# Kernel tuning notes

Measured on AMD Instinct MI355X. Metric: run time of the kernel, lower is better.

## Reference

```python
import jax, jax.numpy as jnp
import numpy as np

N, K, FEAT = 64, 32, 1024      # nodes, neighbors per node, input feature dim
C1, F1 = 4, 16                 # layer1: out_channels=4, out_features=hidden[0]/4=16
C2, F2 = 32, 1                 # layer2: out_channels=hidden[1]=32, out_features=1
NUM_CLASS = 10
BN_EPS = 1e-5


def _sgnroot(x):
    return jnp.sign(x) * jnp.sqrt(jnp.clip(jnp.abs(x), 1e-8))


def _feature_adjacency(x, nb):
    # x: (N,c,f), nb: (N,K,c,f) -> adj: (N,c,f,f)
    fadj = jnp.einsum('nca,nkcb->ncab', x, nb)          # sum over K neighbors
    fadj = fadj + jnp.swapaxes(fadj, -2, -1)
    s = _sgnroot(fadj)
    out = s / (jnp.abs(s).sum(axis=1, keepdims=True) + 1e-7)  # row-normalize over channel dim
    return jnp.where(jnp.isnan(out), 0.0, out)


def _layer(x, nb, W, c_out, f_out):
    # FeatTrans1d.forward: adjacency build + batched matmul + full-width conv (== dense contraction)
    n = x.shape[0]
    adj = _feature_adjacency(x, nb)                     # (N,c,f,f)
    xa = jnp.einsum('ncab,ncb->nca', adj, x)            # adj @ x
    x2 = jnp.einsum('ocf,ncf->no', W, xa).reshape(n, c_out, f_out)
    na = jnp.einsum('ncab,nkcb->nkca', adj, nb)         # per-node adj applied to its neighbors
    nb2 = jnp.einsum('ocf,nkcf->nko', W, na).reshape(n, -1, c_out, f_out)
    return x2, nb2


def _bn_softsign_x(x, w, b):
    # BatchNorm1d (training stats over batch+feature dims) + Softsign; x: (N,C,F)
    m = x.mean(axis=(0, 2), keepdims=True)
    v = x.var(axis=(0, 2), keepdims=True)
    y = (x - m) / jnp.sqrt(v + BN_EPS) * w[None, :, None] + b[None, :, None]
    return y / (1.0 + jnp.abs(y))


def _bn_softsign_nb(x, w, b):
    # each node's neighbor set is normalized independently (list comprehension in original); x: (N,K,C,F)
    m = x.mean(axis=(1, 3), keepdims=True)
    v = x.var(axis=(1, 3), keepdims=True)
    y = (x - m) / jnp.sqrt(v + BN_EPS) * w[None, None, :, None] + b[None, None, :, None]
    return y / (1.0 + jnp.abs(y))


def setup_inputs() -> dict:
    key = jax.random.key(0)
    ks = jax.random.split(key, 6)
    return {
        'x': jax.random.normal(ks[0], (N, 1, FEAT), jnp.float32),
        'neighbor': jax.random.normal(ks[1], (N, K, 1, FEAT), jnp.float32),
        'W1': jax.random.normal(ks[2], (C1 * F1, 1, FEAT), jnp.float32) * (1.0 / FEAT) ** 0.5,
        'W2': jax.random.normal(ks[3], (C2 * F2, C1, F1), jnp.float32) * (1.0 / (C1 * F1)) ** 0.5,
        'bn1_w': jnp.ones((C1,), jnp.float32),
        'bn1_b': jnp.zeros((C1,), jnp.float32),
        'bn2_w': jnp.ones((C2,), jnp.float32),
        'bn2_b': jnp.zeros((C2,), jnp.float32),
        'lin_w': jax.random.normal(ks[4], (NUM_CLASS, C2 * F2), jnp.float32) * (1.0 / (C2 * F2)) ** 0.5,
        'lin_b': jnp.zeros((NUM_CLASS,), jnp.float32),
    }


def reference(x, neighbor, W1, W2, bn1_w, bn1_b, bn2_w, bn2_b, lin_w, lin_b):
    x1, nb1 = _layer(x, neighbor, W1, C1, F1)           # (N,4,16), (N,K,4,16)
    x1 = _bn_softsign_x(x1, bn1_w, bn1_b)
    nb1 = _bn_softsign_nb(nb1, bn1_w, bn1_b)
    x2, _ = _layer(x1, nb1, W2, C2, F2)                 # (N,32,1)
    x2 = _bn_softsign_x(x2, bn2_w, bn2_b)
    return x2.reshape(x2.shape[0], -1) @ lin_w.T + lin_b  # (N,NUM_CLASS)
```

## Files before the change

kernel.cpp:

```cpp
#include <hip/hip_runtime.h>

typedef unsigned short u16;
typedef short short8 __attribute__((ext_vector_type(8)));
typedef float floatx4 __attribute__((ext_vector_type(4)));
typedef float floatx2 __attribute__((ext_vector_type(2)));
typedef unsigned int uintx4 __attribute__((ext_vector_type(4)));
typedef unsigned int uintx2 __attribute__((ext_vector_type(2)));
typedef u16 ushortx4 __attribute__((ext_vector_type(4)));

#define FEAT 1024
#define KNB  32

__device__ __forceinline__ u16 f2bf(float f) {
    unsigned u = __float_as_uint(f);
    u += 0x7fffu + ((u >> 16) & 1u);
    return (u16)(u >> 16);
}
__device__ __forceinline__ unsigned pack2bf(float a, float b) {
    return (unsigned)f2bf(a) | ((unsigned)f2bf(b) << 16);
}
__device__ __forceinline__ float softsign(float v) { return v / (1.f + fabsf(v)); }

union Frag { uintx4 q; unsigned d[4]; short8 v; };

__global__ __launch_bounds__(256, 2) void k2_main(
    const float* __restrict__ xg, const float* __restrict__ nbg,
    const float* __restrict__ w1g, float* __restrict__ pws)
{
    __shared__ float sS[FEAT];
    __shared__ float sX[FEAT];
    __shared__ u16  sY[34 * 1024];

    const int t = threadIdx.x;
    const int n = blockIdx.x >> 3;
    const int chunk = blockIdx.x & 7;
    const int chunkbase = chunk * 128;
    const int w = t >> 6;
    const int l = t & 63;
    const int m = l & 15;
    const int g = l >> 4;

    {
        ushortx4 z4 = {0, 0, 0, 0};
        *(ushortx4*)&sY[33 * 1024 + t * 4] = z4;
    }
    {
        floatx4 xv = *(const floatx4*)(xg + (size_t)n * FEAT + t * 4);
        *(floatx4*)&sX[t * 4] = xv;
        ushortx4 xb4 = {f2bf(xv[0]), f2bf(xv[1]), f2bf(xv[2]), f2bf(xv[3])};
        *(ushortx4*)&sY[t * 4] = xb4;
    }
    {
        const float* nbase = nbg + ((size_t)n * KNB) * FEAT + t * 4;
        floatx4 sacc = {0.f, 0.f, 0.f, 0.f};
        #pragma unroll 4
        for (int k = 0; k < KNB; ++k) {
            floatx4 v = *(const floatx4*)(nbase + (size_t)k * FEAT);
            sacc += v;
            int row = k + 1;
            int c16 = (t >> 1) ^ (row & 7);
            ushortx4 p4 = {f2bf(v[0]), f2bf(v[1]), f2bf(v[2]), f2bf(v[3])};
            *(ushortx4*)&sY[row * 1024 + c16 * 8 + (t & 1) * 4] = p4;
        }
        *(floatx4*)&sS[t * 4] = sacc;
    }

    const float xa0 = xg[(size_t)n * FEAT + chunkbase + w * 32 + m];
    const float xa1 = xg[(size_t)n * FEAT + chunkbase + w * 32 + 16 + m];
    __syncthreads();
    const float Sa0 = sS[chunkbase + w * 32 + m];
    const float Sa1 = sS[chunkbase + w * 32 + 16 + m];

    const u16* b2base = (m == 0) ? &sY[32 * 1024] : &sY[33 * 1024];
    const int sw = (m & 7);

    floatx4 acc[2][3];
    #pragma unroll
    for (int i = 0; i < 2; ++i)
        #pragma unroll
        for (int j = 0; j < 3; ++j) { floatx4 z = {0.f, 0.f, 0.f, 0.f}; acc[i][j] = z; }

    const floatx2 vxa0 = {xa0, xa0}, vxa1 = {xa1, xa1};
    const floatx2 vSa0 = {Sa0, Sa0}, vSa1 = {Sa1, Sa1};

    #pragma unroll 2
    for (int s = 0; s < 32; ++s) {
        const int bloc = s * 32 + g * 8;
        const int cidx = bloc >> 3;

        floatx4 xq0 = *(const floatx4*)&sX[bloc];
        floatx4 xq1 = *(const floatx4*)&sX[bloc + 4];
        floatx4 sq0 = *(const floatx4*)&sS[bloc];
        floatx4 sq1 = *(const floatx4*)&sS[bloc + 4];

        Frag af0, af1;
        #pragma unroll
        for (int p = 0; p < 4; ++p) {
            floatx2 xbp = (p < 2) ? ((p == 0) ? (floatx2){xq0[0], xq0[1]} : (floatx2){xq0[2], xq0[3]})
                                  : ((p == 2) ? (floatx2){xq1[0], xq1[1]} : (floatx2){xq1[2], xq1[3]});
            floatx2 sbp = (p < 2) ? ((p == 0) ? (floatx2){sq0[0], sq0[1]} : (floatx2){sq0[2], sq0[3]})
                                  : ((p == 2) ? (floatx2){sq1[0], sq1[1]} : (floatx2){sq1[2], sq1[3]});
            floatx2 u0 = xbp * vSa0 + sbp * vxa0;
            floatx2 u1 = xbp * vSa1 + sbp * vxa1;
            uintx2 b0b = __builtin_bit_cast(uintx2, u0);
            uintx2 b1b = __builtin_bit_cast(uintx2, u1);
            af0.d[p] = 0x3F803F80u | (b0b.y & 0x80000000u) | ((b0b.x >> 16) & 0x8000u);
            af1.d[p] = 0x3F803F80u | (b1b.y & 0x80000000u) | ((b1b.x >> 16) & 0x8000u);
        }

        Frag b0, b1, b2;
        b0.q = *(const uintx4*)&sY[ m       * 1024 + ((cidx ^ sw) << 3)];
        b1.q = *(const uintx4*)&sY[(16 + m) * 1024 + ((cidx ^ sw) << 3)];
        b2.q = *(const uintx4*)&b2base[cidx << 3];

        acc[0][0] = __builtin_amdgcn_mfma_f32_16x16x32_bf16(af0.v, b0.v, acc[0][0], 0, 0, 0);
        acc[0][1] = __builtin_amdgcn_mfma_f32_16x16x32_bf16(af0.v, b1.v, acc[0][1], 0, 0, 0);
        acc[0][2] = __builtin_amdgcn_mfma_f32_16x16x32_bf16(af0.v, b2.v, acc[0][2], 0, 0, 0);
        acc[1][0] = __builtin_amdgcn_mfma_f32_16x16x32_bf16(af1.v, b0.v, acc[1][0], 0, 0, 0);
        acc[1][1] = __builtin_amdgcn_mfma_f32_16x16x32_bf16(af1.v, b1.v, acc[1][1], 0, 0, 0);
        acc[1][2] = __builtin_amdgcn_mfma_f32_16x16x32_bf16(af1.v, b2.v, acc[1][2], 0, 0, 0);
    }
    __syncthreads();

    u16* sZ = sY;
    #pragma unroll
    for (int ti = 0; ti < 2; ++ti)
        #pragma unroll
        for (int jt = 0; jt < 3; ++jt) {
            int j = jt * 16 + m;
            int aloc = w * 32 + ti * 16 + g * 4;
            ushortx4 zz;
            zz.x = f2bf(acc[ti][jt][0]);
            zz.y = f2bf(acc[ti][jt][1]);
            zz.z = f2bf(acc[ti][jt][2]);
            zz.w = f2bf(acc[ti][jt][3]);
            *(ushortx4*)&sZ[j * 136 + aloc] = zz;
        }
    __syncthreads();

    floatx4 a2[3];
    #pragma unroll
    for (int j = 0; j < 3; ++j) { floatx4 z = {0.f, 0.f, 0.f, 0.f}; a2[j] = z; }
    #pragma unroll
    for (int kc = 0; kc < 4; ++kc) {
        const float* wsrc = w1g + (size_t)(w * 16 + m) * FEAT + chunkbase + kc * 32 + g * 8;
        floatx4 wf0 = *(const floatx4*)wsrc;
        floatx4 wf1 = *(const floatx4*)(wsrc + 4);
        Frag wb;
        wb.d[0] = pack2bf(wf0[0], wf0[1]);
        wb.d[1] = pack2bf(wf0[2], wf0[3]);
        wb.d[2] = pack2bf(wf1[0], wf1[1]);
        wb.d[3] = pack2bf(wf1[2], wf1[3]);
        #pragma unroll
        for (int jt = 0; jt < 3; ++jt) {
            Frag za;
            za.q = *(const uintx4*)&sZ[(jt * 16 + m) * 136 + kc * 32 + g * 8];
            a2[jt] = __builtin_amdgcn_mfma_f32_16x16x32_bf16(za.v, wb.v, a2[jt], 0, 0, 0);
        }
    }
    float* pbase = pws + (size_t)(n * 8 + chunk) * 33 * 64;
    #pragma unroll
    for (int jt = 0; jt < 3; ++jt)
        #pragma unroll
        for (int r = 0; r < 4; ++r) {
            int j = jt * 16 + g * 4 + r;
            if (j < 33) pbase[j * 64 + w * 16 + m] = a2[jt][r];
        }
}

__global__ __launch_bounds__(256, 1) void kB(
    const float* __restrict__ pws, const float* __restrict__ bn1w,
    const float* __restrict__ bn1b, const float* __restrict__ w2g,
    float* __restrict__ x22ws)
{
    __shared__ float sx2[64 * 64];
    __shared__ float snb[32 * 64];
    __shared__ float sx1[64], sS1[64], sadj[4 * 16 * 16], sxa[64];
    __shared__ float ssc[4], sbi[4], ssc2[4], sbi2[4];
    const int t = threadIdx.x;
    const int n = blockIdx.x;

    #pragma unroll
    for (int r = 0; r < 4; ++r) {
        int slot = t + r * 256;
        int nn = slot >> 4, oc = slot & 15;
        const float* p = pws + (size_t)nn * 16896 + oc * 4;
        floatx4 tmp[8];
        #pragma unroll
        for (int c = 0; c < 8; ++c) tmp[c] = *(const floatx4*)(p + c * 2112);
        floatx4 s01 = tmp[0] + tmp[1], s23 = tmp[2] + tmp[3];
        floatx4 s45 = tmp[4] + tmp[5], s67 = tmp[6] + tmp[7];
        *(floatx4*)&sx2[slot * 4] = (s01 + s23) + (s45 + s67);
    }
    #pragma unroll
    for (int r = 0; r < 2; ++r) {
        int slot = t + r * 256;
        int k = slot >> 4, oc = slot & 15;
        const float* p = pws + (size_t)n * 16896 + (1 + k) * 64 + oc * 4;
        floatx4 tmp[8];
        #pragma unroll
        for (int c = 0; c < 8; ++c) tmp[c] = *(const floatx4*)(p + c * 2112);
        floatx4 s01 = tmp[0] + tmp[1], s23 = tmp[2] + tmp[3];
        floatx4 s45 = tmp[4] + tmp[5], s67 = tmp[6] + tmp[7];
        *(floatx4*)&snb[slot * 4] = (s01 + s23) + (s45 + s67);
    }
    __syncthreads();
    {
        int cc = t >> 6, l2 = t & 63;
        float s = 0.f, s2 = 0.f;
        #pragma unroll
        for (int i = 0; i < 16; ++i) {
            int idx = l2 * 16 + i;
            int nn = idx >> 4, f = idx & 15;
            float v = sx2[nn * 64 + cc * 16 + f];
            s += v; s2 += v * v;
        }
        float s3 = 0.f, s4 = 0.f;
        #pragma unroll
        for (int i = 0; i < 8; ++i) {
            int idx = l2 * 8 + i;
            int k = idx >> 4, f = idx & 15;
            float v = snb[k * 64 + cc * 16 + f];
            s3 += v; s4 += v * v;
        }
        #pragma unroll
        for (int off = 32; off > 0; off >>= 1) {
            s  += __shfl_down(s, off);  s2 += __shfl_down(s2, off);
            s3 += __shfl_down(s3, off); s4 += __shfl_down(s4, off);
        }
        if (l2 == 0) {
            float wv = bn1w[cc], bv = bn1b[cc];
            float mean = s * (1.f / 1024.f);
            float var = s2 * (1.f / 1024.f) - mean * mean;
            float rs = rsqrtf(var + 1e-5f);
            ssc[cc] = rs * wv;
            sbi[cc] = bv - mean * rs * wv;
            float mean2 = s3 * (1.f / 512.f);
            float var2 = s4 * (1.f / 512.f) - mean2 * mean2;
            float rs2 = rsqrtf(var2 + 1e-5f);
            ssc2[cc] = rs2 * wv;
            sbi2[cc] = bv - mean2 * rs2 * wv;
        }
    }
    __syncthreads();
    if (t < 64) {
        int cc = t >> 4;
        sx1[t] = softsign(sx2[n * 64 + t] * ssc[cc] + sbi[cc]);
        float a = 0.f;
        for (int k = 0; k < KNB; ++k)
            a += softsign(snb[k * 64 + t] * ssc2[cc] + sbi2[cc]);
        sS1[t] = a;
    }
    __syncthreads();
    {
        int a = t >> 4, b = t & 15;
        float sc[4]; float den = 1e-7f;
        #pragma unroll
        for (int c = 0; c < 4; ++c) {
            float u = sx1[c * 16 + a] * sS1[c * 16 + b] + sx1[c * 16 + b] * sS1[c * 16 + a];
            float r = sqrtf(fmaxf(fabsf(u), 1e-8f));
            sc[c] = copysignf(r, u);
            den += r;
        }
        float inv = 1.f / den;
        #pragma unroll
        for (int c = 0; c < 4; ++c) sadj[(c * 16 + a) * 16 + b] = sc[c] * inv;
    }
    __syncthreads();
    if (t < 64) {
        int cc = t >> 4;
        float a = 0.f;
        #pragma unroll
        for (int b = 0; b < 16; ++b) a += sadj[t * 16 + b] * sx1[cc * 16 + b];
        sxa[t] = a;
    }
    __syncthreads();
    if (t < 32) {
        float a = 0.f;
        #pragma unroll
        for (int cf = 0; cf < 64; ++cf) a += w2g[t * 64 + cf] * sxa[cf];
        x22ws[n * 32 + t] = a;
    }
}

__global__ __launch_bounds__(256) void kC(
    const float* __restrict__ x22ws, const float* __restrict__ bn2w,
    const float* __restrict__ bn2b, const float* __restrict__ linw,
    const float* __restrict__ linb, float* __restrict__ outg)
{
    __shared__ float sy[64 * 32];
    __shared__ float ssc[32], sbi[32];
    __shared__ float sx[64 * 32];
    const int t = threadIdx.x;
    #pragma unroll
    for (int r = 0; r < 8; ++r) sx[t + r * 256] = x22ws[t + r * 256];
    __syncthreads();
    if (t < 32) {
        float s = 0.f, s2 = 0.f;
        for (int nn = 0; nn < 64; ++nn) {
            float v = sx[nn * 32 + t];
            s += v; s2 += v * v;
        }
        float mean = s * (1.f / 64.f);
        float var = s2 * (1.f / 64.f) - mean * mean;
        float rs = rsqrtf(var + 1e-5f);
        float wv = bn2w[t], bv = bn2b[t];
        ssc[t] = rs * wv;
        sbi[t] = bv - mean * rs * wv;
    }
    __syncthreads();
    #pragma unroll
    for (int r = 0; r < 8; ++r) {
        int idx = t + r * 256;
        int o = idx & 31;
        sy[idx] = softsign(sx[idx] * ssc[o] + sbi[o]);
    }
    __syncthreads();
    for (int r = 0; r < 3; ++r) {
        int idx = t + r * 256;
        if (idx < 640) {
            int nn = idx / 10, cls = idx % 10;
            float a = linb[cls];
            #pragma unroll
            for (int o = 0; o < 32; ++o) a += sy[nn * 32 + o] * linw[cls * 32 + o];
            outg[idx] = a;
        }
    }
}

extern "C" void kernel_launch(void* const* d_in, const int* in_sizes, int n_in,
                              void* d_out, int out_size, void* d_ws, size_t ws_size,
                              hipStream_t stream) {
    (void)in_sizes; (void)n_in; (void)out_size; (void)ws_size;
    const float* xg   = (const float*)d_in[0];
    const float* nbg  = (const float*)d_in[1];
    const float* w1g  = (const float*)d_in[2];
    const float* w2g  = (const float*)d_in[3];
    const float* bn1w = (const float*)d_in[4];
    const float* bn1b = (const float*)d_in[5];
    const float* bn2w = (const float*)d_in[6];
    const float* bn2b = (const float*)d_in[7];
    const float* linw = (const float*)d_in[8];
    const float* linb = (const float*)d_in[9];

    float* pws   = (float*)d_ws;
    float* x22ws = pws + (size_t)64 * 8 * 33 * 64;
    float* outg  = (float*)d_out;

    k2_main<<<dim3(512), dim3(256), 0, stream>>>(xg, nbg, w1g, pws);
    kB<<<dim3(64), dim3(256), 0, stream>>>(pws, bn1w, bn1b, w2g, x22ws);
    kC<<<dim3(1), dim3(256), 0, stream>>>(x22ws, bn2w, bn2b, linw, linb, outg);
}
```

Measured before the change: 108.1 us.

## Fuse three kernels into one persistent kernel with atomic grid barriers

Merges the layer-1 MFMA kernel, the per-node layer-2 kernel and the final BN/linear kernel into a single launch. The stages are chained with a global atomic counter barrier that 64 selected blocks spin on, followed by a last-block-done counter that picks one block for the final stage. Shared memory is overlaid through a union so the stages reuse it. The aim is to remove two kernel launch gaps. In exchange it adds a memset launch and relies on all 512 blocks being co-resident, which risks deadlock or spinning overhead.

```diff
diff --git a/kernel.cpp b/kernel.cpp
--- a/kernel.cpp
+++ b/kernel.cpp
@@ -23,17 +23,44 @@
 
 union Frag { uintx4 q; unsigned d[4]; short8 v; };
 
-__global__ __launch_bounds__(256, 2) void k2_main(
+union SMem {
+    struct {
+        float sS[FEAT];
+        float sX[FEAT];
+        u16   sY[34 * 1024];
+    } p1;
+    struct {
+        float sx2[64 * 64];
+        float snb[32 * 64];
+        float sx1[64], sS1[64], sadj[4 * 16 * 16], sxa[64];
+        float ssc[4], sbi[4], ssc2[4], sbi2[4];
+        int   flag;
+    } p2;
+    struct {
+        float sy[64 * 32];
+        float sx[64 * 32];
+        float ssc[32], sbi[32];
+    } p3;
+};
+
+__global__ __launch_bounds__(256, 2) void k_mega(
     const float* __restrict__ xg, const float* __restrict__ nbg,
-    const float* __restrict__ w1g, float* __restrict__ pws)
+    const float* __restrict__ w1g, const float* __restrict__ w2g,
+    const float* __restrict__ bn1w, const float* __restrict__ bn1b,
+    const float* __restrict__ bn2w, const float* __restrict__ bn2b,
+    const float* __restrict__ linw, const float* __restrict__ linb,
+    float* __restrict__ pws, float* __restrict__ x22ws,
+    unsigned int* __restrict__ cnt, float* __restrict__ outg)
 {
-    __shared__ float sS[FEAT];
-    __shared__ float sX[FEAT];
-    __shared__ u16  sY[34 * 1024];
+    __shared__ SMem sm;
+    float* const sS = sm.p1.sS;
+    float* const sX = sm.p1.sX;
+    u16*   const sY = sm.p1.sY;
 
     const int t = threadIdx.x;
-    const int n = blockIdx.x >> 3;
-    const int chunk = blockIdx.x & 7;
+    const int bid = blockIdx.x;
+    const int n = bid >> 3;
+    const int chunk = bid & 7;
     const int chunkbase = chunk * 128;
     const int w = t >> 6;
     const int l = t & 63;
@@ -166,19 +193,30 @@
             int j = jt * 16 + g * 4 + r;
             if (j < 33) pbase[j * 64 + w * 16 + m] = a2[jt][r];
         }
-}
-
-__global__ __launch_bounds__(256, 1) void kB(
-    const float* __restrict__ pws, const float* __restrict__ bn1w,
-    const float* __restrict__ bn1b, const float* __restrict__ w2g,
-    float* __restrict__ x22ws)
-{
-    __shared__ float sx2[64 * 64];
-    __shared__ float snb[32 * 64];
-    __shared__ float sx1[64], sS1[64], sadj[4 * 16 * 16], sxa[64];
-    __shared__ float ssc[4], sbi[4], ssc2[4], sbi2[4];
-    const int t = threadIdx.x;
-    const int n = blockIdx.x;
+
+    __threadfence();
+    __syncthreads();
+    if (t == 0) atomicAdd(&cnt[0], 1u);
+
+    if ((bid & 7) != (n & 7)) return;
+
+    if (t == 0) {
+        while (__hip_atomic_load(&cnt[0], __ATOMIC_ACQUIRE, __HIP_MEMORY_SCOPE_AGENT) < 512u)
+            __builtin_amdgcn_s_sleep(2);
+    }
+    __syncthreads();
+    __threadfence();
+
+    float* const sx2  = sm.p2.sx2;
+    float* const snb  = sm.p2.snb;
+    float* const sx1  = sm.p2.sx1;
+    float* const sS1  = sm.p2.sS1;
+    float* const sadj = sm.p2.sadj;
+    float* const sxa  = sm.p2.sxa;
+    float* const ssc  = sm.p2.ssc;
+    float* const sbi  = sm.p2.sbi;
+    float* const ssc2 = sm.p2.ssc2;
+    float* const sbi2 = sm.p2.sbi2;
 
     #pragma unroll
     for (int r = 0; r < 4; ++r) {
@@ -281,39 +319,41 @@
         for (int cf = 0; cf < 64; ++cf) a += w2g[t * 64 + cf] * sxa[cf];
         x22ws[n * 32 + t] = a;
     }
-}
-
-__global__ __launch_bounds__(256) void kC(
-    const float* __restrict__ x22ws, const float* __restrict__ bn2w,
-    const float* __restrict__ bn2b, const float* __restrict__ linw,
-    const float* __restrict__ linb, float* __restrict__ outg)
-{
-    __shared__ float sy[64 * 32];
-    __shared__ float ssc[32], sbi[32];
-    __shared__ float sx[64 * 32];
-    const int t = threadIdx.x;
-    #pragma unroll
-    for (int r = 0; r < 8; ++r) sx[t + r * 256] = x22ws[t + r * 256];
+
+    __threadfence();
+    __syncthreads();
+    if (t == 0) sm.p2.flag = (int)atomicAdd(&cnt[1], 1u);
+    __syncthreads();
+    if (sm.p2.flag != 63) return;
+    __threadfence();
+
+    float* const sy   = sm.p3.sy;
+    float* const sx3  = sm.p3.sx;
+    float* const ssc3 = sm.p3.ssc;
+    float* const sbi3 = sm.p3.sbi;
+
+    #pragma unroll
+    for (int r = 0; r < 8; ++r) sx3[t + r * 256] = x22ws[t + r * 256];
     __syncthreads();
     if (t < 32) {
         float s = 0.f, s2 = 0.f;
         for (int nn = 0; nn < 64; ++nn) {
-            float v = sx[nn * 32 + t];
+            float v = sx3[nn * 32 + t];
             s += v; s2 += v * v;
         }
         float mean = s * (1.f / 64.f);
         float var = s2 * (1.f / 64.f) - mean * mean;
         float rs = rsqrtf(var + 1e-5f);
         float wv = bn2w[t], bv = bn2b[t];
-        ssc[t] = rs * wv;
-        sbi[t] = bv - mean * rs * wv;
+        ssc3[t] = rs * wv;
+        sbi3[t] = bv - mean * rs * wv;
     }
     __syncthreads();
     #pragma unroll
     for (int r = 0; r < 8; ++r) {
         int idx = t + r * 256;
         int o = idx & 31;
-        sy[idx] = softsign(sx[idx] * ssc[o] + sbi[o]);
+        sy[idx] = softsign(sx3[idx] * ssc3[o] + sbi3[o]);
     }
     __syncthreads();
     for (int r = 0; r < 3; ++r) {
@@ -345,9 +385,11 @@
 
     float* pws   = (float*)d_ws;
     float* x22ws = pws + (size_t)64 * 8 * 33 * 64;
+    unsigned int* cnt = (unsigned int*)(x22ws + 64 * 32);
     float* outg  = (float*)d_out;
 
-    k2_main<<<dim3(512), dim3(256), 0, stream>>>(xg, nbg, w1g, pws);
-    kB<<<dim3(64), dim3(256), 0, stream>>>(pws, bn1w, bn1b, w2g, x22ws);
-    kC<<<dim3(1), dim3(256), 0, stream>>>(x22ws, bn2w, bn2b, linw, linb, outg);
+    hipMemsetAsync(cnt, 0, 64, stream);
+    k_mega<<<dim3(512), dim3(256), 0, stream>>>(xg, nbg, w1g, w2g, bn1w, bn1b,
+                                                bn2w, bn2b, linw, linb,
+                                                pws, x22ws, cnt, outg);
 }
```

Measured after the change: 172.5 us. 59.5% more time.

## Split feature contraction dimension in half across blocks to double grid and occupancy

Applied to the files above, without the earlier changes.

The main kernel now splits the 1024-wide reduction over b into two halves, each handled by a separate block. The launch grows to 1024 blocks, shared memory per block is halved, and launch bounds rise to 4 blocks per CU. The per-row neighbor sum for the block's own chunk is computed separately, and the partial-sum reduction in the second kernel now combines 16 partials per node instead of 8. The goal is better latency hiding and more CU utilisation, at the cost of twice the partial-result workspace traffic and redundant loads of W1 and the neighbor data.

```diff
diff --git a/kernel.cpp b/kernel.cpp
--- a/kernel.cpp
+++ b/kernel.cpp
@@ -23,55 +23,60 @@
 
 union Frag { uintx4 q; unsigned d[4]; short8 v; };
 
-__global__ __launch_bounds__(256, 2) void k2_main(
+__global__ __launch_bounds__(256, 4) void k2_main(
     const float* __restrict__ xg, const float* __restrict__ nbg,
     const float* __restrict__ w1g, float* __restrict__ pws)
 {
-    __shared__ float sS[FEAT];
-    __shared__ float sX[FEAT];
-    __shared__ u16  sY[34 * 1024];
+    __shared__ float sS[512];
+    __shared__ float sX[512];
+    __shared__ float sSa[128];
+    __shared__ u16  sY[34 * 512];
 
     const int t = threadIdx.x;
-    const int n = blockIdx.x >> 3;
-    const int chunk = blockIdx.x & 7;
+    const int bid = blockIdx.x;
+    const int n = bid >> 4;
+    const int h = (bid >> 3) & 1;
+    const int chunk = bid & 7;
     const int chunkbase = chunk * 128;
+    const int hbase = h * 512;
     const int w = t >> 6;
     const int l = t & 63;
     const int m = l & 15;
     const int g = l >> 4;
 
-    {
-        ushortx4 z4 = {0, 0, 0, 0};
-        *(ushortx4*)&sY[33 * 1024 + t * 4] = z4;
-    }
-    {
-        floatx4 xv = *(const floatx4*)(xg + (size_t)n * FEAT + t * 4);
+    if (t < 64) { uintx4 z = {0, 0, 0, 0}; *(uintx4*)&sY[33 * 512 + t * 8] = z; }
+    if (t < 128) {
+        floatx4 xv = *(const floatx4*)(xg + (size_t)n * FEAT + hbase + t * 4);
         *(floatx4*)&sX[t * 4] = xv;
         ushortx4 xb4 = {f2bf(xv[0]), f2bf(xv[1]), f2bf(xv[2]), f2bf(xv[3])};
         *(ushortx4*)&sY[t * 4] = xb4;
+        const float* ap = nbg + ((size_t)n * KNB) * FEAT + chunkbase + t;
+        float sa = 0.f;
+        #pragma unroll
+        for (int k = 0; k < KNB; ++k) sa += ap[(size_t)k * FEAT];
+        sSa[t] = sa;
     }
     {
-        const float* nbase = nbg + ((size_t)n * KNB) * FEAT + t * 4;
-        floatx4 sacc = {0.f, 0.f, 0.f, 0.f};
-        #pragma unroll 4
+        const float* nbase = nbg + ((size_t)n * KNB) * FEAT + hbase + t * 2;
+        floatx2 sacc = {0.f, 0.f};
+        #pragma unroll 8
         for (int k = 0; k < KNB; ++k) {
-            floatx4 v = *(const floatx4*)(nbase + (size_t)k * FEAT);
+            floatx2 v = *(const floatx2*)(nbase + (size_t)k * FEAT);
             sacc += v;
             int row = k + 1;
-            int c16 = (t >> 1) ^ (row & 7);
-            ushortx4 p4 = {f2bf(v[0]), f2bf(v[1]), f2bf(v[2]), f2bf(v[3])};
-            *(ushortx4*)&sY[row * 1024 + c16 * 8 + (t & 1) * 4] = p4;
-        }
-        *(floatx4*)&sS[t * 4] = sacc;
+            int c16 = (t >> 2) ^ (row & 7);
+            *(unsigned*)&sY[row * 512 + c16 * 8 + (t & 3) * 2] = pack2bf(v.x, v.y);
+        }
+        *(floatx2*)&sS[t * 2] = sacc;
     }
 
     const float xa0 = xg[(size_t)n * FEAT + chunkbase + w * 32 + m];
     const float xa1 = xg[(size_t)n * FEAT + chunkbase + w * 32 + 16 + m];
     __syncthreads();
-    const float Sa0 = sS[chunkbase + w * 32 + m];
-    const float Sa1 = sS[chunkbase + w * 32 + 16 + m];
-
-    const u16* b2base = (m == 0) ? &sY[32 * 1024] : &sY[33 * 1024];
+    const float Sa0 = sSa[w * 32 + m];
+    const float Sa1 = sSa[w * 32 + 16 + m];
+
+    const u16* b2base = (m == 0) ? &sY[32 * 512] : &sY[33 * 512];
     const int sw = (m & 7);
 
     floatx4 acc[2][3];
@@ -84,7 +89,7 @@
     const floatx2 vSa0 = {Sa0, Sa0}, vSa1 = {Sa1, Sa1};
 
     #pragma unroll 2
-    for (int s = 0; s < 32; ++s) {
+    for (int s = 0; s < 16; ++s) {
         const int bloc = s * 32 + g * 8;
         const int cidx = bloc >> 3;
 
@@ -109,8 +114,8 @@
         }
 
         Frag b0, b1, b2;
-        b0.q = *(const uintx4*)&sY[ m       * 1024 + ((cidx ^ sw) << 3)];
-        b1.q = *(const uintx4*)&sY[(16 + m) * 1024 + ((cidx ^ sw) << 3)];
+        b0.q = *(const uintx4*)&sY[ m       * 512 + ((cidx ^ sw) << 3)];
+        b1.q = *(const uintx4*)&sY[(16 + m) * 512 + ((cidx ^ sw) << 3)];
         b2.q = *(const uintx4*)&b2base[cidx << 3];
 
         acc[0][0] = __builtin_amdgcn_mfma_f32_16x16x32_bf16(af0.v, b0.v, acc[0][0], 0, 0, 0);
@@ -158,7 +163,7 @@
             a2[jt] = __builtin_amdgcn_mfma_f32_16x16x32_bf16(za.v, wb.v, a2[jt], 0, 0, 0);
         }
     }
-    float* pbase = pws + (size_t)(n * 8 + chunk) * 33 * 64;
+    float* pbase = pws + (size_t)(n * 16 + h * 8 + chunk) * 33 * 64;
     #pragma unroll
     for (int jt = 0; jt < 3; ++jt)
         #pragma unroll
@@ -184,25 +189,31 @@
     for (int r = 0; r < 4; ++r) {
         int slot = t + r * 256;
         int nn = slot >> 4, oc = slot & 15;
-        const float* p = pws + (size_t)nn * 16896 + oc * 4;
-        floatx4 tmp[8];
-        #pragma unroll
-        for (int c = 0; c < 8; ++c) tmp[c] = *(const floatx4*)(p + c * 2112);
-        floatx4 s01 = tmp[0] + tmp[1], s23 = tmp[2] + tmp[3];
-        floatx4 s45 = tmp[4] + tmp[5], s67 = tmp[6] + tmp[7];
-        *(floatx4*)&sx2[slot * 4] = (s01 + s23) + (s45 + s67);
+        const float* p = pws + (size_t)nn * 33792 + oc * 4;
+        floatx4 a0 = {0,0,0,0}, a1 = {0,0,0,0}, a2 = {0,0,0,0}, a3 = {0,0,0,0};
+        #pragma unroll
+        for (int c = 0; c < 4; ++c) {
+            a0 += *(const floatx4*)(p + c * 2112);
+            a1 += *(const floatx4*)(p + (4 + c) * 2112);
+            a2 += *(const floatx4*)(p + (8 + c) * 2112);
+            a3 += *(const floatx4*)(p + (12 + c) * 2112);
+        }
+        *(floatx4*)&sx2[slot * 4] = (a0 + a1) + (a2 + a3);
     }
     #pragma unroll
     for (int r = 0; r < 2; ++r) {
         int slot = t + r * 256;
         int k = slot >> 4, oc = slot & 15;
-        const float* p = pws + (size_t)n * 16896 + (1 + k) * 64 + oc * 4;
-        floatx4 tmp[8];
-        #pragma unroll
-        for (int c = 0; c < 8; ++c) tmp[c] = *(const floatx4*)(p + c * 2112);
-        floatx4 s01 = tmp[0] + tmp[1], s23 = tmp[2] + tmp[3];
-        floatx4 s45 = tmp[4] + tmp[5], s67 = tmp[6] + tmp[7];
-        *(floatx4*)&snb[slot * 4] = (s01 + s23) + (s45 + s67);
+        const float* p = pws + (size_t)n * 33792 + (1 + k) * 64 + oc * 4;
+        floatx4 a0 = {0,0,0,0}, a1 = {0,0,0,0}, a2 = {0,0,0,0}, a3 = {0,0,0,0};
+        #pragma unroll
+        for (int c = 0; c < 4; ++c) {
+            a0 += *(const floatx4*)(p + c * 2112);
+            a1 += *(const floatx4*)(p + (4 + c) * 2112);
+            a2 += *(const floatx4*)(p + (8 + c) * 2112);
+            a3 += *(const floatx4*)(p + (12 + c) * 2112);
+        }
+        *(floatx4*)&snb[slot * 4] = (a0 + a1) + (a2 + a3);
     }
     __syncthreads();
     {
@@ -344,10 +355,10 @@
     const float* linb = (const float*)d_in[9];
 
     float* pws   = (float*)d_ws;
-    float* x22ws = pws + (size_t)64 * 8 * 33 * 64;
+    float* x22ws = pws + (size_t)64 * 16 * 33 * 64;
     float* outg  = (float*)d_out;
 
-    k2_main<<<dim3(512), dim3(256), 0, stream>>>(xg, nbg, w1g, pws);
+    k2_main<<<dim3(1024), dim3(256), 0, stream>>>(xg, nbg, w1g, pws);
     kB<<<dim3(64), dim3(256), 0, stream>>>(pws, bn1w, bn1b, w2g, x22ws);
     kC<<<dim3(1), dim3(256), 0, stream>>>(x22ws, bn2w, bn2b, linw, linb, outg);
 }
```

Result: slower. 113.0 us (+4.5%).
